# Performance work log

Measured on AMD Instinct MI355X. Metric: run time of the kernel, lower is better.

## Reference

```python
import jax, jax.numpy as jnp
import numpy as np
import math

B, S, D_MODEL, N_HEADS = 4, 2048, 1024, 16
D_HEAD = D_MODEL // N_HEADS

def _xavier(key, shape, gain):
    # nn.init.xavier_uniform_ on [n_heads, fan_in, fan_out]: fan from last two dims
    fan_in, fan_out = shape[-2], shape[-1]
    bound = gain * math.sqrt(6.0 / (fan_in + fan_out))
    return jax.random.uniform(key, shape, jnp.float32, -bound, bound)

def setup_inputs() -> dict:
    key = jax.random.key(0)
    ks = jax.random.split(key, 5)
    g = 1.0 / math.sqrt(2.0)
    return {
        "x": jax.random.normal(ks[0], (B, S, D_MODEL), jnp.float32),
        "W_Q": _xavier(ks[1], (N_HEADS, D_MODEL, D_HEAD), g),
        "W_K": _xavier(ks[2], (N_HEADS, D_MODEL, D_HEAD), g),
        "W_V": _xavier(ks[3], (N_HEADS, D_MODEL, D_HEAD), g),
        "W_O": _xavier(ks[4], (N_HEADS, D_HEAD, D_MODEL), 1.0),
        "b_Q": jnp.zeros((N_HEADS, D_HEAD), jnp.float32),
        "b_K": jnp.zeros((N_HEADS, D_HEAD), jnp.float32),
        "b_V": jnp.zeros((N_HEADS, D_HEAD), jnp.float32),
        "b_O": jnp.zeros((D_MODEL,), jnp.float32),
    }

def reference(x, W_Q, W_K, W_V, W_O, b_Q, b_K, b_V, b_O):
    # q,k,v: [b, s, h, d_head]
    q = jnp.einsum('bsd,hde->bshe', x, W_Q) + b_Q
    k = jnp.einsum('bsd,hde->bshe', x, W_K) + b_K
    v = jnp.einsum('bsd,hde->bshe', x, W_V) + b_V
    scores = jnp.einsum('bqhe,bkhe->bhqk', q, k) / jnp.sqrt(jnp.float32(D_HEAD))
    attn = jax.nn.softmax(scores, axis=-1)  # [b, h, q, k]
    v_out = jnp.einsum('bkhe,bhqk->bqhe', v, attn)
    return jnp.einsum('bqhe,hed->bqd', v_out, W_O) + b_O
```

## Files before the change

kernel.cpp:

```cpp
#include <hip/hip_runtime.h>
#include <hip/hip_bf16.h>
#include <cmath>

#define B_ 4
#define S_ 2048
#define DM_ 1024
#define H_ 16
#define DH_ 64
#define BS_ (B_*S_)

typedef __bf16 bf16x8 __attribute__((ext_vector_type(8)));
typedef __bf16 bf16x4 __attribute__((ext_vector_type(4)));
typedef float  floatx4 __attribute__((ext_vector_type(4)));

__device__ __forceinline__ void gl_lds16(const __bf16* g, __bf16* l) {
  __builtin_amdgcn_global_load_lds(
      (const __attribute__((address_space(1))) void*)g,
      (__attribute__((address_space(3))) void*)l, 16, 0, 0);
}

__global__ void transpose_kernel(const float* __restrict__ src, __bf16* __restrict__ dst,
                                 int R, int C, long srcBatch, long dstBatch) {
  __shared__ __bf16 tile[32][33];
  int b = blockIdx.z;
  long sb = (long)b * srcBatch;
  dst += (long)b * dstBatch;
  int c0 = blockIdx.x * 32, r0 = blockIdx.y * 32;
  int tx = threadIdx.x, ty = threadIdx.y;
  #pragma unroll
  for (int i = 0; i < 32; i += 8)
    tile[ty + i][tx] = (__bf16)src[sb + (long)(r0 + ty + i) * C + (c0 + tx)];
  __syncthreads();
  #pragma unroll
  for (int i = 0; i < 32; i += 8)
    dst[(long)(c0 + ty + i) * R + (r0 + tx)] = tile[tx][ty + i];
}

__global__ void transpose_qkv_kernel(const float* __restrict__ WQ,
                                     const float* __restrict__ WK,
                                     const float* __restrict__ WV,
                                     __bf16* __restrict__ dst) {
  __shared__ __bf16 tile[32][33];
  int z = blockIdx.z;
  int mat = z >> 4, head = z & 15;
  const float* src = (mat == 0 ? WQ : (mat == 1 ? WK : WV)) + (long)head * 65536;
  dst += (long)mat * 1048576 + (long)head * 65536;
  int c0 = blockIdx.x * 32, r0 = blockIdx.y * 32;
  int tx = threadIdx.x, ty = threadIdx.y;
  #pragma unroll
  for (int i = 0; i < 32; i += 8)
    tile[ty + i][tx] = (__bf16)src[(long)(r0 + ty + i) * 64 + (c0 + tx)];
  __syncthreads();
  #pragma unroll
  for (int i = 0; i < 32; i += 8)
    dst[(long)(c0 + ty + i) * 1024 + (r0 + tx)] = tile[tx][ty + i];
}

__global__ void cvt_kernel(const float* __restrict__ src, __bf16* __restrict__ dst) {
  long i = ((long)blockIdx.x * 256 + threadIdx.x) * 8;
  float4 a = *(const float4*)(src + i);
  float4 b = *(const float4*)(src + i + 4);
  bf16x8 t;
  t[0] = (__bf16)a.x; t[1] = (__bf16)a.y; t[2] = (__bf16)a.z; t[3] = (__bf16)a.w;
  t[4] = (__bf16)b.x; t[5] = (__bf16)b.y; t[6] = (__bf16)b.z; t[7] = (__bf16)b.w;
  *(bf16x8*)(dst + i) = t;
}

#define BM 128
#define BN 128
#define BK 64

template<int EPI>
__global__ __launch_bounds__(256, 4) void gemm_kernel(
    const __bf16* __restrict__ A, const __bf16* __restrict__ Bt,
    int M, int N, int K,
    const float* __restrict__ bq, const float* __restrict__ bk,
    const float* __restrict__ bv, const float* __restrict__ bo,
    __bf16* __restrict__ q_ws, __bf16* __restrict__ k_ws,
    __bf16* __restrict__ vT_ws, float* __restrict__ out) {

  __shared__ __align__(16) __bf16 smem[17408];
  __bf16* As = smem;
  __bf16* Bs = smem + 8192;

  int tid  = threadIdx.x;
  int wave = tid >> 6, lane = tid & 63;
  int quad = lane >> 4, l15 = lane & 15;
  int wm = (wave >> 1) * 64, wn = (wave & 1) * 64;

  int nbx = gridDim.x;
  int lid = blockIdx.y * nbx + blockIdx.x;
  int cpx = (nbx * gridDim.y) >> 3;
  int sid = (lid & 7) * cpx + (lid >> 3);
  long m0 = (long)(sid / nbx) * BM;
  long n0 = (long)(sid % nbx) * BN;

  floatx4 acc[4][4] = {};

  int r  = tid >> 3, c8 = tid & 7;
  int cx = c8 ^ (r & 7);
  const __bf16* Asrc = A  + (m0 + r) * (long)K + cx * 8;
  const __bf16* Bsrc = Bt + (n0 + r) * (long)K + cx * 8;

#define STAGE(k0) do {                                                       \
    _Pragma("unroll")                                                        \
    for (int i = 0; i < 4; i++) {                                            \
      gl_lds16(Asrc + (long)(i * 32) * K + (k0), &As[(i * 256 + tid) * 8]);  \
      gl_lds16(Bsrc + (long)(i * 32) * K + (k0), &Bs[(i * 256 + tid) * 8]);  \
    }                                                                        \
  } while (0)

  int swz = l15 & 7;
  const int NT = K / BK;

  STAGE(0);

  for (int t = 0; t < NT; ++t) {
    __syncthreads();

    #pragma unroll
    for (int kk = 0; kk < 2; kk++) {
      bf16x8 af[4], bff[4];
      #pragma unroll
      for (int mt = 0; mt < 4; mt++)
        af[mt] = *(const bf16x8*)(&As[(wm + mt * 16 + l15) * 64 + (((kk * 4 + quad) ^ swz) * 8)]);
      #pragma unroll
      for (int nt = 0; nt < 4; nt++)
        bff[nt] = *(const bf16x8*)(&Bs[(wn + nt * 16 + l15) * 64 + (((kk * 4 + quad) ^ swz) * 8)]);
      #pragma unroll
      for (int mt = 0; mt < 4; mt++)
        #pragma unroll
        for (int nt = 0; nt < 4; nt++)
          acc[mt][nt] = __builtin_amdgcn_mfma_f32_16x16x32_bf16(af[mt], bff[nt], acc[mt][nt], 0, 0, 0);
    }

    if (t + 1 < NT) {
      __syncthreads();
      STAGE((t + 1) * BK);
    }
  }
#undef STAGE

  if (EPI == 0) {
    int seg = (int)(n0 >> 10);
    if (seg < 2) {
      #pragma unroll
      for (int nt = 0; nt < 4; nt++) {
        long n = n0 + wn + nt * 16 + l15;
        int he  = (int)(n & 1023);
        int h = he >> 6, e = he & 63;
        const float* bias = (seg == 0 ? bq : bk);
        float bval = bias[he];
        float scale = (seg == 0 ? 0.125f * 1.44269504088896340f : 1.0f);
        __bf16* dst0 = (seg == 0 ? q_ws : k_ws);
        #pragma unroll
        for (int mt = 0; mt < 4; mt++) {
          #pragma unroll
          for (int rr = 0; rr < 4; rr++) {
            long m = m0 + wm + mt * 16 + quad * 4 + rr;
            int b = (int)(m >> 11), s = (int)(m & 2047);
            float v = (acc[mt][nt][rr] + bval) * scale;
            dst0[((long)(b * 16 + h) * 2048 + s) * 64 + e] = (__bf16)v;
          }
        }
      }
    } else {
      __syncthreads();
      __bf16* vl = smem + wave * 4352;
      #pragma unroll
      for (int nt = 0; nt < 4; nt++) {
        long n = n0 + wn + nt * 16 + l15;
        float bval = bv[(int)(n & 1023)];
        #pragma unroll
        for (int mt = 0; mt < 4; mt++) {
          bf16x4 pw;
          #pragma unroll
          for (int rr = 0; rr < 4; rr++) pw[rr] = (__bf16)(acc[mt][nt][rr] + bval);
          *(bf16x4*)(&vl[(nt * 16 + l15) * 68 + mt * 16 + quad * 4]) = pw;
        }
      }
      asm volatile("s_waitcnt lgkmcnt(0)" ::: "memory");
      int bb = (int)((m0 + wm) >> 11), s0 = (int)((m0 + wm) & 2047);
      #pragma unroll
      for (int rep = 0; rep < 2; rep++) {
        int j = (lane >> 1) + rep * 32;
        long n = n0 + wn + j;
        int he = (int)(n & 1023);
        int h = he >> 6, e = he & 63;
        __bf16* dst = vT_ws + ((long)(bb * 16 + h) * 64 + e) * 2048 + s0 + (lane & 1) * 32;
        const __bf16* srcl = &vl[j * 68 + (lane & 1) * 32];
        #pragma unroll
        for (int c = 0; c < 4; c++)
          *(bf16x8*)(dst + c * 8) = *(const bf16x8*)(srcl + c * 8);
      }
    }
  } else {
    #pragma unroll
    for (int mt = 0; mt < 4; mt++) {
      #pragma unroll
      for (int rr = 0; rr < 4; rr++) {
        long m = m0 + wm + mt * 16 + quad * 4 + rr;
        #pragma unroll
        for (int nt = 0; nt < 4; nt++) {
          long n = n0 + wn + nt * 16 + l15;
          out[m * N + n] = acc[mt][nt][rr] + bo[n];
        }
      }
    }
  }
}

#define KBLK 64

__global__ __launch_bounds__(256, 2) void attn_kernel(
    const __bf16* __restrict__ Q, const __bf16* __restrict__ Kk,
    const __bf16* __restrict__ Vt, __bf16* __restrict__ vout) {

  __shared__ __align__(16) __bf16 Kb[2][64 * 64];
  __shared__ __align__(16) __bf16 Vb[2][64 * 64];
  __shared__ __align__(16) __bf16 Pb[4][16 * 64];

  int tid = threadIdx.x, wave = tid >> 6, lane = tid & 63;
  int quad = lane >> 4, l15 = lane & 15;

  int id = blockIdx.x;
  int xcd = id & 7, rest = id >> 3;
  int qt = rest & 7, bhhi = rest >> 3;
  int bh = bhhi * 8 + xcd;
  int b = bh >> 4, h = bh & 15;
  int q0 = qt * 256 + wave * 64;

  const __bf16* Qbh = Q  + (long)(b * 16 + h) * 2048 * 64;
  const __bf16* Kbh = Kk + (long)(b * 16 + h) * 2048 * 64;
  const __bf16* Vbh = Vt + (long)(b * 16 + h) * 64 * 2048;

  int rs0 = tid >> 3, cc0 = tid & 7;
  int ccs = cc0 ^ (rs0 & 7);
  const __bf16* Ksrc0 = Kbh + (long)rs0 * 64 + ccs * 8;
  const __bf16* Ksrc1 = Kbh + (long)(rs0 + 32) * 64 + ccs * 8;
  const __bf16* Vsrc0 = Vbh + (long)rs0 * 2048 + ccs * 8;
  const __bf16* Vsrc1 = Vbh + (long)(rs0 + 32) * 2048 + ccs * 8;

#define STAGE(buf, kb) do {                                   \
    gl_lds16(Ksrc0 + (long)(kb) * 64, &Kb[buf][tid * 8]);      \
    gl_lds16(Ksrc1 + (long)(kb) * 64, &Kb[buf][tid * 8 + 2048]); \
    gl_lds16(Vsrc0 + (kb),            &Vb[buf][tid * 8]);      \
    gl_lds16(Vsrc1 + (kb),            &Vb[buf][tid * 8 + 2048]); \
  } while (0)

  bf16x8 qf[4][2];
  #pragma unroll
  for (int qh = 0; qh < 4; qh++)
    #pragma unroll
    for (int t = 0; t < 2; t++)
      qf[qh][t] = *(const bf16x8*)(Qbh + (long)(q0 + qh * 16 + l15) * 64 + t * 32 + quad * 8);

  floatx4 o[4][4] = {};
  floatx4 ol[4] = {};
  bf16x8 onesv;
  #pragma unroll
  for (int j = 0; j < 8; j++) onesv[j] = (__bf16)1.0f;

  int swz = l15 & 7;

  STAGE(0, 0);

  for (int kb = 0; kb < 2048; kb += KBLK) {
    int cur = (kb >> 6) & 1;

    __syncthreads();
    if (kb + KBLK < 2048) STAGE(cur ^ 1, kb + KBLK);

    floatx4 sc[4][4];
    __builtin_amdgcn_s_setprio(1);
    #pragma unroll
    for (int nt = 0; nt < 4; nt++) {
      const __bf16* kp = &Kb[cur][(nt * 16 + l15) * 64];
      bf16x8 k0 = *(const bf16x8*)(kp + ((0 + quad) ^ swz) * 8);
      bf16x8 k1 = *(const bf16x8*)(kp + ((4 + quad) ^ swz) * 8);
      #pragma unroll
      for (int qh = 0; qh < 4; qh++) {
        floatx4 z = { 0.f, 0.f, 0.f, 0.f };
        z = __builtin_amdgcn_mfma_f32_16x16x32_bf16(k0, qf[qh][0], z, 0, 0, 0);
        sc[qh][nt] = __builtin_amdgcn_mfma_f32_16x16x32_bf16(k1, qf[qh][1], z, 0, 0, 0);
      }
    }
    __builtin_amdgcn_s_setprio(0);

    bf16x8 vf[2][4];
    #pragma unroll
    for (int t = 0; t < 2; t++)
      #pragma unroll
      for (int dn = 0; dn < 4; dn++)
        vf[t][dn] = *(const bf16x8*)(&Vb[cur][(dn * 16 + l15) * 64 + ((t * 4 + quad) ^ swz) * 8]);

    #pragma unroll
    for (int qh = 0; qh < 4; qh++) {
      #pragma unroll
      for (int nt = 0; nt < 4; nt++) {
        bf16x4 pw;
        #pragma unroll
        for (int rr = 0; rr < 4; rr++)
          pw[rr] = (__bf16)__builtin_amdgcn_exp2f(sc[qh][nt][rr]);
        *(bf16x4*)(&Pb[wave][l15 * 64 + (((nt * 2 + (quad >> 1)) ^ swz) * 8) + (quad & 1) * 4]) = pw;
      }

      __builtin_amdgcn_s_setprio(1);
      #pragma unroll
      for (int t = 0; t < 2; t++) {
        bf16x8 pf = *(const bf16x8*)(&Pb[wave][l15 * 64 + ((t * 4 + quad) ^ swz) * 8]);
        ol[qh] = __builtin_amdgcn_mfma_f32_16x16x32_bf16(onesv, pf, ol[qh], 0, 0, 0);
        #pragma unroll
        for (int dn = 0; dn < 4; dn++)
          o[qh][dn] = __builtin_amdgcn_mfma_f32_16x16x32_bf16(vf[t][dn], pf, o[qh][dn], 0, 0, 0);
      }
      __builtin_amdgcn_s_setprio(0);
    }
  }
#undef STAGE

  #pragma unroll
  for (int qh = 0; qh < 4; qh++) {
    float rl = 1.f / ol[qh][0];
    int s = q0 + qh * 16 + l15;
    __bf16* outr = vout + ((long)(b * 2048 + s) * 16 + h) * 64;
    #pragma unroll
    for (int dn = 0; dn < 4; dn++) {
      bf16x4 w;
      #pragma unroll
      for (int rr = 0; rr < 4; rr++) w[rr] = (__bf16)(o[qh][dn][rr] * rl);
      *(bf16x4*)(outr + dn * 16 + quad * 4) = w;
    }
  }
}

extern "C" void kernel_launch(void* const* d_in, const int* in_sizes, int n_in,
                              void* d_out, int out_size, void* d_ws, size_t ws_size,
                              hipStream_t stream) {
  const float* x  = (const float*)d_in[0];
  const float* WQ = (const float*)d_in[1];
  const float* WK = (const float*)d_in[2];
  const float* WV = (const float*)d_in[3];
  const float* WO = (const float*)d_in[4];
  const float* bq = (const float*)d_in[5];
  const float* bk = (const float*)d_in[6];
  const float* bv = (const float*)d_in[7];
  const float* bo = (const float*)d_in[8];
  float* out = (float*)d_out;

  uint8_t* ws = (uint8_t*)d_ws;
  const long MB16 = 16777216;
  __bf16* q_ws  = (__bf16*)(ws);
  __bf16* k_ws  = (__bf16*)(ws + 1 * MB16);
  __bf16* vT_ws = (__bf16*)(ws + 2 * MB16);
  __bf16* Wt    = (__bf16*)(ws + 3 * MB16);
  __bf16* vout  = (__bf16*)(ws + 3 * MB16);
  __bf16* WOt   = (__bf16*)(ws);
  __bf16* xb    = (__bf16*)d_out;

  dim3 tb(32, 8);
  transpose_qkv_kernel<<<dim3(2, 32, 48), tb, 0, stream>>>(WQ, WK, WV, Wt);

  cvt_kernel<<<dim3(4096), 256, 0, stream>>>(x, xb);

  gemm_kernel<0><<<dim3(3072 / BN, 8192 / BM), 256, 0, stream>>>(
      xb, Wt, BS_, 3072, DM_, bq, bk, bv, nullptr, q_ws, k_ws, vT_ws, nullptr);

  attn_kernel<<<dim3(512), 256, 0, stream>>>(q_ws, k_ws, vT_ws, vout);

  transpose_kernel<<<dim3(32, 32, 1), tb, 0, stream>>>(WO, WOt, 1024, 1024, 0, 0);

  gemm_kernel<1><<<dim3(1024 / BN, 8192 / BM), 256, 0, stream>>>(
      vout, WOt, BS_, DM_, DM_, nullptr, nullptr, nullptr, bo, nullptr, nullptr, nullptr, out);
}
```

Before: 275.8 us.

## Halve attention block size and single-buffer K tile to raise occupancy

The attention kernel now uses 128-thread blocks (2 waves, 128 queries) and launches twice as many blocks. The K tile is single-buffered and the next K block is loaded after a mid-iteration barrier once QK^T is done, while V stays double-buffered. This cuts LDS per block so more blocks can be resident per CU. In exchange it adds an extra barrier per iteration, exposes K load latency, and each block reloads K/V for fewer queries, which doubles global K/V traffic.

```diff
diff --git a/kernel.cpp b/kernel.cpp
--- a/kernel.cpp
+++ b/kernel.cpp
@@ -212,23 +212,23 @@
 
 #define KBLK 64
 
-__global__ __launch_bounds__(256, 2) void attn_kernel(
+__global__ __launch_bounds__(128, 2) void attn_kernel(
     const __bf16* __restrict__ Q, const __bf16* __restrict__ Kk,
     const __bf16* __restrict__ Vt, __bf16* __restrict__ vout) {
 
-  __shared__ __align__(16) __bf16 Kb[2][64 * 64];
+  __shared__ __align__(16) __bf16 Kb[64 * 64];
   __shared__ __align__(16) __bf16 Vb[2][64 * 64];
-  __shared__ __align__(16) __bf16 Pb[4][16 * 64];
+  __shared__ __align__(16) __bf16 Pb[2][16 * 64];
 
   int tid = threadIdx.x, wave = tid >> 6, lane = tid & 63;
   int quad = lane >> 4, l15 = lane & 15;
 
   int id = blockIdx.x;
   int xcd = id & 7, rest = id >> 3;
-  int qt = rest & 7, bhhi = rest >> 3;
+  int qt = rest & 15, bhhi = rest >> 4;
   int bh = bhhi * 8 + xcd;
   int b = bh >> 4, h = bh & 15;
-  int q0 = qt * 256 + wave * 64;
+  int q0 = qt * 128 + wave * 64;
 
   const __bf16* Qbh = Q  + (long)(b * 16 + h) * 2048 * 64;
   const __bf16* Kbh = Kk + (long)(b * 16 + h) * 2048 * 64;
@@ -236,16 +236,20 @@
 
   int rs0 = tid >> 3, cc0 = tid & 7;
   int ccs = cc0 ^ (rs0 & 7);
-  const __bf16* Ksrc0 = Kbh + (long)rs0 * 64 + ccs * 8;
-  const __bf16* Ksrc1 = Kbh + (long)(rs0 + 32) * 64 + ccs * 8;
-  const __bf16* Vsrc0 = Vbh + (long)rs0 * 2048 + ccs * 8;
-  const __bf16* Vsrc1 = Vbh + (long)(rs0 + 32) * 2048 + ccs * 8;
-
-#define STAGE(buf, kb) do {                                   \
-    gl_lds16(Ksrc0 + (long)(kb) * 64, &Kb[buf][tid * 8]);      \
-    gl_lds16(Ksrc1 + (long)(kb) * 64, &Kb[buf][tid * 8 + 2048]); \
-    gl_lds16(Vsrc0 + (kb),            &Vb[buf][tid * 8]);      \
-    gl_lds16(Vsrc1 + (kb),            &Vb[buf][tid * 8 + 2048]); \
+  const __bf16* Ksrc = Kbh + (long)rs0 * 64 + ccs * 8;
+  const __bf16* Vsrc = Vbh + (long)rs0 * 2048 + ccs * 8;
+
+#define STAGE_K(kb) do {                                             \
+    _Pragma("unroll")                                                \
+    for (int i = 0; i < 4; i++)                                      \
+      gl_lds16(Ksrc + (long)(kb) * 64 + (long)(16 * i) * 64,         \
+               &Kb[(tid + 128 * i) * 8]);                            \
+  } while (0)
+#define STAGE_V(buf, kb) do {                                        \
+    _Pragma("unroll")                                                \
+    for (int i = 0; i < 4; i++)                                      \
+      gl_lds16(Vsrc + (kb) + (long)(16 * i) * 2048,                  \
+               &Vb[buf][(tid + 128 * i) * 8]);                       \
   } while (0)
 
   bf16x8 qf[4][2];
@@ -263,19 +267,20 @@
 
   int swz = l15 & 7;
 
-  STAGE(0, 0);
+  STAGE_K(0);
+  STAGE_V(0, 0);
 
   for (int kb = 0; kb < 2048; kb += KBLK) {
     int cur = (kb >> 6) & 1;
 
     __syncthreads();
-    if (kb + KBLK < 2048) STAGE(cur ^ 1, kb + KBLK);
+    if (kb + KBLK < 2048) STAGE_V(cur ^ 1, kb + KBLK);
 
     floatx4 sc[4][4];
     __builtin_amdgcn_s_setprio(1);
     #pragma unroll
     for (int nt = 0; nt < 4; nt++) {
-      const __bf16* kp = &Kb[cur][(nt * 16 + l15) * 64];
+      const __bf16* kp = &Kb[(nt * 16 + l15) * 64];
       bf16x8 k0 = *(const bf16x8*)(kp + ((0 + quad) ^ swz) * 8);
       bf16x8 k1 = *(const bf16x8*)(kp + ((4 + quad) ^ swz) * 8);
       #pragma unroll
@@ -287,6 +292,10 @@
     }
     __builtin_amdgcn_s_setprio(0);
 
+    asm volatile("s_waitcnt lgkmcnt(0)" ::: "memory");
+    __builtin_amdgcn_s_barrier();
+    if (kb + KBLK < 2048) STAGE_K(kb + KBLK);
+
     bf16x8 vf[2][4];
     #pragma unroll
     for (int t = 0; t < 2; t++)
@@ -317,7 +326,8 @@
       __builtin_amdgcn_s_setprio(0);
     }
   }
-#undef STAGE
+#undef STAGE_K
+#undef STAGE_V
 
   #pragma unroll
   for (int qh = 0; qh < 4; qh++) {
@@ -366,7 +376,7 @@
   gemm_kernel<0><<<dim3(3072 / BN, 8192 / BM), 256, 0, stream>>>(
       xb, Wt, BS_, 3072, DM_, bq, bk, bv, nullptr, q_ws, k_ws, vT_ws, nullptr);
 
-  attn_kernel<<<dim3(512), 256, 0, stream>>>(q_ws, k_ws, vT_ws, vout);
+  attn_kernel<<<dim3(1024), 128, 0, stream>>>(q_ws, k_ws, vT_ws, vout);
 
   transpose_kernel<<<dim3(32, 32, 1), tb, 0, stream>>>(WO, WOt, 1024, 1024, 0, 0);
 
```

Result: no change. 274.9 us (-0.3%).
